# Kernel tuning notes

Measured on AMD Instinct MI355X. Metric: run time of the kernel, lower is better.

The kernel has to match this reference:

```python
import jax, jax.numpy as jnp
import numpy as np

DIM = 256
HEADS = 8
WS = 8            # window size
SHIFT = 4
MLP_HID = 1024
EPS = 1e-5
HEAD_DIM = DIM // HEADS
SCALE = HEAD_DIM ** -0.5
N = WS * WS       # tokens per window


def _rel_pos_index():
    coords = np.stack(np.meshgrid(np.arange(WS), np.arange(WS), indexing='ij'))  # [2,ws,ws]
    flat = coords.reshape(2, -1)                                                  # [2,N]
    rel = flat[:, :, None] - flat[:, None, :]                                     # [2,N,N]
    rel = rel.transpose(1, 2, 0)                                                  # [N,N,2]
    rel[:, :, 0] += WS - 1
    rel[:, :, 1] += WS - 1
    rel[:, :, 0] *= 2 * WS - 1
    return jnp.asarray(rel.sum(-1))                                               # [N,N] int

REL_IDX = _rel_pos_index()


def layernorm(x, g, b):
    mu = x.mean(-1, keepdims=True)
    var = ((x - mu) ** 2).mean(-1, keepdims=True)
    return (x - mu) * jax.lax.rsqrt(var + EPS) * g + b


def setup_inputs() -> dict:
    key = jax.random.key(0)
    ks = jax.random.split(key, 16)
    s = 0.02
    return {
        'x': jax.random.normal(ks[0], (16, 16384, DIM), jnp.float32),
        'qkv_w': jax.random.normal(ks[1], (DIM, 3 * DIM), jnp.float32) * s,
        'qkv_b': jnp.zeros((3 * DIM,), jnp.float32),
        'proj_w': jax.random.normal(ks[2], (DIM, DIM), jnp.float32) * s,
        'proj_b': jnp.zeros((DIM,), jnp.float32),
        'rpb_table': jax.random.normal(ks[3], ((2 * WS - 1) ** 2, HEADS), jnp.float32) * s,
        'ln1_g': jnp.ones((DIM,), jnp.float32),
        'ln1_b': jnp.zeros((DIM,), jnp.float32),
        'ln2_g': jnp.ones((DIM,), jnp.float32),
        'ln2_b': jnp.zeros((DIM,), jnp.float32),
        'mlp_w1': jax.random.normal(ks[4], (DIM, MLP_HID), jnp.float32) * s,
        'mlp_b1': jnp.zeros((MLP_HID,), jnp.float32),
        'mlp_w2': jax.random.normal(ks[5], (MLP_HID, DIM), jnp.float32) * s,
        'mlp_b2': jnp.zeros((DIM,), jnp.float32),
        'H': 128,
        'W': 128,
    }


def reference(x, qkv_w, qkv_b, proj_w, proj_b, rpb_table,
              ln1_g, ln1_b, ln2_g, ln2_b, mlp_w1, mlp_b1, mlp_w2, mlp_b2, H, W):
    B, L, C = x.shape
    shortcut = x

    h = layernorm(x, ln1_g, ln1_b).reshape(B, H, W, C)
    if SHIFT > 0:
        h = jnp.roll(h, (-SHIFT, -SHIFT), axis=(1, 2))

    # window partition: [B,H,W,C] -> [B*nW, N, C]
    h = h.reshape(B, H // WS, WS, W // WS, WS, C).transpose(0, 1, 3, 2, 4, 5)
    xw = h.reshape(-1, N, C)
    Bw = xw.shape[0]

    # window attention
    qkv = (xw @ qkv_w + qkv_b).reshape(Bw, N, 3, HEADS, HEAD_DIM)
    q, k, v = qkv[:, :, 0], qkv[:, :, 1], qkv[:, :, 2]        # [Bw,N,H,D]
    attn = jnp.einsum('bnhd,bmhd->bhnm', q, k) * SCALE         # [Bw,H,N,N]
    bias = rpb_table[REL_IDX.reshape(-1)].reshape(N, N, HEADS).transpose(2, 0, 1)
    attn = jax.nn.softmax(attn + bias[None], axis=-1)
    out = jnp.einsum('bhnm,bmhd->bnhd', attn, v).reshape(Bw, N, C)
    out = out @ proj_w + proj_b

    # window reverse
    out = out.reshape(B, H // WS, W // WS, WS, WS, C).transpose(0, 1, 3, 2, 4, 5).reshape(B, H, W, C)
    if SHIFT > 0:
        out = jnp.roll(out, (SHIFT, SHIFT), axis=(1, 2))
    out = out.reshape(B, L, C)

    h2 = layernorm(out, ln2_g, ln2_b)
    mlp = jax.nn.gelu(h2 @ mlp_w1 + mlp_b1, approximate=False) @ mlp_w2 + mlp_b2
    return shortcut + out + mlp
```

## Files before the change

kernel.cpp:

```cpp
#include <hip/hip_runtime.h>
#include <math.h>

typedef short bfrag __attribute__((ext_vector_type(8)));
typedef float ffrag __attribute__((ext_vector_type(4)));

#define MFMA16(a, b, c) __builtin_amdgcn_mfma_f32_16x16x32_bf16((a), (b), (c), 0, 0, 0)

__device__ __align__(16) unsigned short g_wt[786432];

__device__ __forceinline__ unsigned bf16b(float f) {
  unsigned u = __float_as_uint(f);
  return (u + 0x7FFFu + ((u >> 16) & 1u)) >> 16;
}
__device__ __forceinline__ unsigned pk2(float lo, float hi) {
  return bf16b(lo) | (bf16b(hi) << 16);
}

__global__ void conv_w(const float* __restrict__ qkv_w, const float* __restrict__ proj_w,
                       const float* __restrict__ w1, const float* __restrict__ w2) {
  const int idx = blockIdx.x * 256 + threadIdx.x;
  const float* src; int c, k2, C, K, ofs;
  if (idx < 98304)       { src = qkv_w;  C = 768;  K = 256;  c = idx % 768;  k2 = idx / 768;  ofs = 0; }
  else if (idx < 131072) { int i = idx - 98304;  src = proj_w; C = 256;  K = 256;  c = i % 256;  k2 = i / 256;  ofs = 196608; }
  else if (idx < 262144) { int i = idx - 131072; src = w1;     C = 1024; K = 256;  c = i % 1024; k2 = i / 1024; ofs = 262144; }
  else                   { int i = idx - 262144; src = w2;     C = 256;  K = 1024; c = i % 256;  k2 = i / 256;  ofs = 524288; }
  const float lo = src[(2 * k2) * C + c];
  const float hi = src[(2 * k2 + 1) * C + c];
  *(unsigned*)&g_wt[ofs + c * K + 2 * k2] = pk2(lo, hi);
}

__device__ __forceinline__ int swz(int row, int col, int C) {
  return row * (C * 2) + ((((col >> 3) ^ (row & 7)) << 4) + ((col & 7) << 1));
}

__device__ __forceinline__ bfrag ldfrag(const char* lds, int outer, int k0, int C) {
  const int l = threadIdx.x & 63;
  return *(const bfrag*)(lds + swz(outer + (l & 15), k0 + ((l >> 4) << 3), C));
}

template <int DSTROWB>
__device__ __forceinline__ void glds_stage(char* lds, const unsigned short* src,
                                           int srcRowShorts, int bytes) {
  const int wv = threadIdx.x >> 6, l = threadIdx.x & 63;
  for (int base = wv * 1024; base < bytes; base += 8192) {
    const int off = base + l * 16;
    const int row = off / DSTROWB;
    const int slot = (off % DSTROWB) >> 4;
    const int sslot = slot ^ (row & 7);
    const unsigned short* g = src + row * srcRowShorts + sslot * 8;
    __builtin_amdgcn_global_load_lds((const __attribute__((address_space(1))) void*)g,
                                     (__attribute__((address_space(3))) void*)(lds + base),
                                     16, 0, 0);
  }
}

__device__ __forceinline__ void ln_row_to_lds(char* dst, const float* __restrict__ src,
                                              const float* __restrict__ g,
                                              const float* __restrict__ bb, int r) {
  const int lane = threadIdx.x & 63;
  const float4 v = *(const float4*)(src + lane * 4);
  float s = v.x + v.y + v.z + v.w;
  #pragma unroll
  for (int o = 32; o; o >>= 1) s += __shfl_xor(s, o);
  const float mu = s * (1.f / 256.f);
  const float d0 = v.x - mu, d1 = v.y - mu, d2 = v.z - mu, d3 = v.w - mu;
  float q = d0 * d0 + d1 * d1 + d2 * d2 + d3 * d3;
  #pragma unroll
  for (int o = 32; o; o >>= 1) q += __shfl_xor(q, o);
  float rs = rsqrtf(q * (1.f / 256.f) + 1e-5f);
  rs = rs * (1.5f - 0.5f * (q * (1.f / 256.f) + 1e-5f) * rs * rs);
  const float4 g4 = *(const float4*)(g + lane * 4);
  const float4 b4 = *(const float4*)(bb + lane * 4);
  const int c = lane * 4;
  *(unsigned*)(dst + swz(r, c, 256)) = pk2(d0 * rs * g4.x + b4.x, d1 * rs * g4.y + b4.y);
  *(unsigned*)(dst + swz(r, c + 2, 256)) = pk2(d2 * rs * g4.z + b4.z, d3 * rs * g4.w + b4.w);
}

__global__ __launch_bounds__(512) void swin_attn(
    const float* __restrict__ x,
    const float* __restrict__ qkv_b, const float* __restrict__ proj_b,
    const float* __restrict__ rpb,
    const float* __restrict__ ln1g, const float* __restrict__ ln1b,
    float* __restrict__ outw)
{
  __shared__ __align__(16) char smem[147456];
  char* XW = smem;
  char* WS = smem + 32768;
  char* QL = smem + 49152;
  char* KL = smem + 81920;
  char* VT = smem + 114688;

  const int t = threadIdx.x;
  const int wv = t >> 6, l = t & 63;
  const int blk = blockIdx.x;
  const int b = blk >> 8, w = blk & 255;
  const int wi = w >> 4, wj = w & 15;

  #pragma unroll
  for (int i = 0; i < 8; ++i) {
    const int r = wv * 8 + i;
    const int ui = (wi * 8 + (r >> 3) + 4) & 127;
    const int uj = (wj * 8 + (r & 7) + 4) & 127;
    const long row = ((long)b << 14) + (ui << 7) + uj;
    ln_row_to_lds(XW, x + row * 256, ln1g, ln1b, r);
  }
  __syncthreads();

  const int MB = (wv >> 2) << 4;
  const int NB = (wv & 3) << 4;
  const float SC = 0.17677669529663687f;

  for (int ch = 0; ch < 24; ++ch) {
    glds_stage<512>(WS, g_wt + ch * 32 * 256, 256, 16384);
    __syncthreads();
    ffrag acc = {0.f, 0.f, 0.f, 0.f};
    #pragma unroll
    for (int ks = 0; ks < 8; ++ks) {
      const bfrag a = ldfrag(WS, MB, ks * 32, 256);
      const bfrag bb = ldfrag(XW, NB, ks * 32, 256);
      acc = MFMA16(a, bb, acc);
    }
    const int r = NB + (l & 15);
    const int cg = ch * 32 + MB + ((l >> 4) << 2);
    const float4 b4 = *(const float4*)(qkv_b + cg);
    float v0 = acc.x + b4.x, v1 = acc.y + b4.y, v2 = acc.z + b4.z, v3 = acc.w + b4.w;
    if (cg < 256) {
      v0 *= SC; v1 *= SC; v2 *= SC; v3 *= SC;
      *(unsigned*)(QL + swz(r, cg, 256)) = pk2(v0, v1);
      *(unsigned*)(QL + swz(r, cg + 2, 256)) = pk2(v2, v3);
    } else if (cg < 512) {
      const int c = cg - 256;
      *(unsigned*)(KL + swz(r, c, 256)) = pk2(v0, v1);
      *(unsigned*)(KL + swz(r, c + 2, 256)) = pk2(v2, v3);
    } else {
      const int c = cg - 512;
      *(unsigned short*)(VT + swz(c + 0, r, 64)) = (unsigned short)bf16b(v0);
      *(unsigned short*)(VT + swz(c + 1, r, 64)) = (unsigned short)bf16b(v1);
      *(unsigned short*)(VT + swz(c + 2, r, 64)) = (unsigned short)bf16b(v2);
      *(unsigned short*)(VT + swz(c + 3, r, 64)) = (unsigned short)bf16b(v3);
    }
    __syncthreads();
  }

  const int w4 = wv & 3;
  const int half = wv >> 2;
  for (int hp = 0; hp < 4; ++hp) {
    const int h = hp * 2 + half;
    char* PB = WS + half * 8192;
    const int hk = h * 32;

    const bfrag aq = ldfrag(QL, w4 * 16, hk, 256);
    ffrag s[4];
    #pragma unroll
    for (int nt = 0; nt < 4; ++nt) {
      const bfrag bk = ldfrag(KL, nt * 16, hk, 256);
      ffrag z = {0.f, 0.f, 0.f, 0.f};
      s[nt] = MFMA16(aq, bk, z);
    }
    const int colb = l & 15;
    const int rbase = w4 * 16 + ((l >> 4) << 2);
    float pr[4][4], mx[4], sm[4];
    #pragma unroll
    for (int reg = 0; reg < 4; ++reg) mx[reg] = -3e38f;
    #pragma unroll
    for (int nt = 0; nt < 4; ++nt) {
      #pragma unroll
      for (int reg = 0; reg < 4; ++reg) {
        const int rr = rbase + reg, cc = nt * 16 + colb;
        const int idx = ((rr >> 3) - (cc >> 3) + 7) * 15 + ((rr & 7) - (cc & 7) + 7);
        pr[nt][reg] = s[nt][reg] + rpb[idx * 8 + h];
        mx[reg] = fmaxf(mx[reg], pr[nt][reg]);
      }
    }
    #pragma unroll
    for (int reg = 0; reg < 4; ++reg) {
      #pragma unroll
      for (int o = 1; o < 16; o <<= 1) mx[reg] = fmaxf(mx[reg], __shfl_xor(mx[reg], o));
      sm[reg] = 0.f;
    }
    #pragma unroll
    for (int nt = 0; nt < 4; ++nt)
      #pragma unroll
      for (int reg = 0; reg < 4; ++reg) {
        pr[nt][reg] = __expf(pr[nt][reg] - mx[reg]);
        sm[reg] += pr[nt][reg];
      }
    #pragma unroll
    for (int reg = 0; reg < 4; ++reg) {
      #pragma unroll
      for (int o = 1; o < 16; o <<= 1) sm[reg] += __shfl_xor(sm[reg], o);
      sm[reg] = 1.f / sm[reg];
    }
    #pragma unroll
    for (int nt = 0; nt < 4; ++nt)
      #pragma unroll
      for (int reg = 0; reg < 4; ++reg)
        *(unsigned short*)(PB + swz(rbase + reg, nt * 16 + colb, 64)) =
            (unsigned short)bf16b(pr[nt][reg] * sm[reg]);
    __syncthreads();

    ffrag o0 = {0.f, 0.f, 0.f, 0.f}, o1 = {0.f, 0.f, 0.f, 0.f};
    #pragma unroll
    for (int ks = 0; ks < 2; ++ks) {
      const bfrag ap = ldfrag(PB, w4 * 16, ks * 32, 64);
      const bfrag bv0 = ldfrag(VT, hk, ks * 32, 64);
      const bfrag bv1 = ldfrag(VT, hk + 16, ks * 32, 64);
      o0 = MFMA16(ap, bv0, o0);
      o1 = MFMA16(ap, bv1, o1);
    }
    #pragma unroll
    for (int reg = 0; reg < 4; ++reg) {
      *(unsigned short*)(XW + swz(rbase + reg, hk + colb, 256)) = (unsigned short)bf16b(o0[reg]);
      *(unsigned short*)(XW + swz(rbase + reg, hk + 16 + colb, 256)) = (unsigned short)bf16b(o1[reg]);
    }
    __syncthreads();
  }

  for (int ch = 0; ch < 8; ++ch) {
    glds_stage<512>(WS, g_wt + 196608 + ch * 32 * 256, 256, 16384);
    __syncthreads();
    ffrag acc = {0.f, 0.f, 0.f, 0.f};
    #pragma unroll
    for (int ks = 0; ks < 8; ++ks) {
      const bfrag a = ldfrag(WS, MB, ks * 32, 256);
      const bfrag bo = ldfrag(XW, NB, ks * 32, 256);
      acc = MFMA16(a, bo, acc);
    }
    const int r = NB + (l & 15);
    const int c0 = ch * 32 + MB + ((l >> 4) << 2);
    const float4 pb4 = *(const float4*)(proj_b + c0);
    const int ui = (wi * 8 + (r >> 3) + 4) & 127;
    const int uj = (wj * 8 + (r & 7) + 4) & 127;
    const long row = ((long)b << 14) + (ui << 7) + uj;
    float4 o4;
    o4.x = acc.x + pb4.x; o4.y = acc.y + pb4.y;
    o4.z = acc.z + pb4.z; o4.w = acc.w + pb4.w;
    *(float4*)(outw + row * 256 + c0) = o4;
    __syncthreads();
  }
}

__global__ __launch_bounds__(512, 4) void swin_mlp(
    const float* __restrict__ x, const float* __restrict__ outw,
    const float* __restrict__ ln2g, const float* __restrict__ ln2b,
    const float* __restrict__ b1, const float* __restrict__ b2,
    float* __restrict__ y)
{
  __shared__ __align__(16) char smem[73728];
  char* H2 = smem;
  char* WS = smem + 32768;
  char* HD = smem + 65536;
  const int t = threadIdx.x, wv = t >> 6, l = t & 63;
  const long base = (long)blockIdx.x << 6;

  #pragma unroll
  for (int i = 0; i < 8; ++i) {
    const int r = wv * 8 + i;
    ln_row_to_lds(H2, outw + (base + r) * 256, ln2g, ln2b, r);
  }
  __syncthreads();

  const int mq = wv >> 1;
  const int nq = (wv & 1) << 1;

  ffrag acc2[2][4];
  {
    ffrag z = {0.f, 0.f, 0.f, 0.f};
    #pragma unroll
    for (int mt = 0; mt < 2; ++mt)
      #pragma unroll
      for (int nt = 0; nt < 4; ++nt) acc2[mt][nt] = z;
  }

  for (int ch = 0; ch < 16; ++ch) {
    glds_stage<512>(WS, g_wt + 262144 + ch * 64 * 256, 256, 32768);
    __syncthreads();
    ffrag a1[2];
    {
      ffrag z = {0.f, 0.f, 0.f, 0.f};
      a1[0] = z; a1[1] = z;
    }
    #pragma unroll
    for (int ks = 0; ks < 8; ++ks) {
      const bfrag a = ldfrag(WS, mq * 16, ks * 32, 256);
      const bfrag bb0 = ldfrag(H2, nq * 16, ks * 32, 256);
      const bfrag bb1 = ldfrag(H2, (nq + 1) * 16, ks * 32, 256);
      a1[0] = MFMA16(a, bb0, a1[0]);
      a1[1] = MFMA16(a, bb1, a1[1]);
    }
    __syncthreads();

    const int c0 = mq * 16 + ((l >> 4) << 2);
    const float4 b14 = *(const float4*)(b1 + ch * 64 + c0);
    #pragma unroll
    for (int nt = 0; nt < 2; ++nt) {
      const int rr = (nq + nt) * 16 + (l & 15);
      const float u0 = a1[nt][0] + b14.x, u1 = a1[nt][1] + b14.y;
      const float u2 = a1[nt][2] + b14.z, u3 = a1[nt][3] + b14.w;
      const float g0 = 0.5f * u0 * (1.f + erff(u0 * 0.70710678118654752f));
      const float g1 = 0.5f * u1 * (1.f + erff(u1 * 0.70710678118654752f));
      const float g2 = 0.5f * u2 * (1.f + erff(u2 * 0.70710678118654752f));
      const float g3 = 0.5f * u3 * (1.f + erff(u3 * 0.70710678118654752f));
      *(unsigned*)(HD + swz(rr, c0, 64)) = pk2(g0, g1);
      *(unsigned*)(HD + swz(rr, c0 + 2, 64)) = pk2(g2, g3);
    }
    glds_stage<128>(WS, g_wt + 524288 + ch * 64, 1024, 32768);
    __syncthreads();

    #pragma unroll
    for (int ks = 0; ks < 2; ++ks) {
      const bfrag am0 = ldfrag(WS, (wv * 2) * 16, ks * 32, 64);
      const bfrag am1 = ldfrag(WS, (wv * 2 + 1) * 16, ks * 32, 64);
      #pragma unroll
      for (int nt = 0; nt < 4; ++nt) {
        const bfrag bb = ldfrag(HD, nt * 16, ks * 32, 64);
        acc2[0][nt] = MFMA16(am0, bb, acc2[0][nt]);
        acc2[1][nt] = MFMA16(am1, bb, acc2[1][nt]);
      }
    }
    __syncthreads();
  }

  #pragma unroll
  for (int mt = 0; mt < 2; ++mt) {
    const int c0 = (wv * 2 + mt) * 16 + ((l >> 4) << 2);
    const float4 b24 = *(const float4*)(b2 + c0);
    #pragma unroll
    for (int nt = 0; nt < 4; ++nt) {
      const long row = base + nt * 16 + (l & 15);
      const float4 xv = *(const float4*)(x + row * 256 + c0);
      const float4 ov = *(const float4*)(outw + row * 256 + c0);
      float4 res;
      res.x = xv.x + ov.x + acc2[mt][nt][0] + b24.x;
      res.y = xv.y + ov.y + acc2[mt][nt][1] + b24.y;
      res.z = xv.z + ov.z + acc2[mt][nt][2] + b24.z;
      res.w = xv.w + ov.w + acc2[mt][nt][3] + b24.w;
      *(float4*)(y + row * 256 + c0) = res;
    }
  }
}

extern "C" void kernel_launch(void* const* d_in, const int* in_sizes, int n_in,
                              void* d_out, int out_size, void* d_ws, size_t ws_size,
                              hipStream_t stream) {
  (void)in_sizes; (void)n_in; (void)out_size; (void)ws_size;
  const float* x      = (const float*)d_in[0];
  const float* qkv_w  = (const float*)d_in[1];
  const float* qkv_b  = (const float*)d_in[2];
  const float* proj_w = (const float*)d_in[3];
  const float* proj_b = (const float*)d_in[4];
  const float* rpb    = (const float*)d_in[5];
  const float* ln1g   = (const float*)d_in[6];
  const float* ln1b   = (const float*)d_in[7];
  const float* ln2g   = (const float*)d_in[8];
  const float* ln2b   = (const float*)d_in[9];
  const float* b1     = (const float*)d_in[11];
  const float* w2     = (const float*)d_in[12];
  const float* b2     = (const float*)d_in[13];
  const float* w1     = (const float*)d_in[10];
  float* y    = (float*)d_out;
  float* outw = (float*)d_ws;

  hipLaunchKernelGGL(conv_w, dim3(1536), dim3(256), 0, stream, qkv_w, proj_w, w1, w2);
  hipLaunchKernelGGL(swin_attn, dim3(4096), dim3(512), 0, stream,
                     x, qkv_b, proj_b, rpb, ln1g, ln1b, outw);
  hipLaunchKernelGGL(swin_mlp, dim3(4096), dim3(512), 0, stream,
                     x, outw, ln2g, ln2b, b1, b2, y);
}
```

Baseline: 1.426 ms.

## Split fused window attention into LN1, QKV GEMM, attention core and projection kernels

```diff
diff --git a/kernel.cpp b/kernel.cpp
--- a/kernel.cpp
+++ b/kernel.cpp
@@ -14,6 +14,9 @@
 }
 __device__ __forceinline__ unsigned pk2(float lo, float hi) {
   return bf16b(lo) | (bf16b(hi) << 16);
+}
+__device__ __forceinline__ float bf2f(unsigned u) {
+  return __uint_as_float(u << 16);
 }
 
 __global__ void conv_w(const float* __restrict__ qkv_w, const float* __restrict__ proj_w,
@@ -32,10 +35,25 @@
 __device__ __forceinline__ int swz(int row, int col, int C) {
   return row * (C * 2) + ((((col >> 3) ^ (row & 7)) << 4) + ((col & 7) << 1));
 }
-
 __device__ __forceinline__ bfrag ldfrag(const char* lds, int outer, int k0, int C) {
   const int l = threadIdx.x & 63;
   return *(const bfrag*)(lds + swz(outer + (l & 15), k0 + ((l >> 4) << 3), C));
+}
+
+__device__ __forceinline__ void stage_tile(char* lds, const unsigned short* __restrict__ src,
+                                           long rowBase, int strideShorts, int kOfs) {
+  const int wv = threadIdx.x >> 6, l = threadIdx.x & 63;
+  #pragma unroll
+  for (int p = 0; p < 8; ++p) {
+    const int base = wv * 1024 + p * 8192;
+    const int off = base + l * 16;
+    const int row = off >> 9;
+    const int ss = ((off & 511) >> 4) ^ (row & 7);
+    const unsigned short* g = src + (rowBase + row) * (long)strideShorts + kOfs + ss * 8;
+    __builtin_amdgcn_global_load_lds((const __attribute__((address_space(1))) void*)g,
+                                     (__attribute__((address_space(3))) void*)(lds + base),
+                                     16, 0, 0);
+  }
 }
 
 template <int DSTROWB>
@@ -46,124 +64,188 @@
     const int off = base + l * 16;
     const int row = off / DSTROWB;
     const int slot = (off % DSTROWB) >> 4;
-    const int sslot = slot ^ (row & 7);
-    const unsigned short* g = src + row * srcRowShorts + sslot * 8;
+    const int ss = slot ^ (row & 7);
+    const unsigned short* g = src + row * srcRowShorts + ss * 8;
     __builtin_amdgcn_global_load_lds((const __attribute__((address_space(1))) void*)g,
                                      (__attribute__((address_space(3))) void*)(lds + base),
                                      16, 0, 0);
   }
 }
 
-__device__ __forceinline__ void ln_row_to_lds(char* dst, const float* __restrict__ src,
-                                              const float* __restrict__ g,
-                                              const float* __restrict__ bb, int r) {
-  const int lane = threadIdx.x & 63;
-  const float4 v = *(const float4*)(src + lane * 4);
-  float s = v.x + v.y + v.z + v.w;
+__device__ __forceinline__ void mm_core(const char* AX, const char* BW, ffrag acc[2][4]) {
+  const int wv = threadIdx.x >> 6;
+  const int rh = wv >> 2, cq = wv & 3;
+  #pragma unroll
+  for (int ks = 0; ks < 8; ++ks) {
+    const bfrag aw0 = ldfrag(BW, cq * 32, ks * 32, 256);
+    const bfrag aw1 = ldfrag(BW, cq * 32 + 16, ks * 32, 256);
+    #pragma unroll
+    for (int nt = 0; nt < 4; ++nt) {
+      const bfrag xb = ldfrag(AX, rh * 64 + nt * 16, ks * 32, 256);
+      acc[0][nt] = MFMA16(aw0, xb, acc[0][nt]);
+      acc[1][nt] = MFMA16(aw1, xb, acc[1][nt]);
+    }
+  }
+}
+
+__device__ __forceinline__ void ln_pack(float d0, float d1, float d2, float d3,
+                                        const float* g, const float* bb, int lane,
+                                        unsigned& o0, unsigned& o1) {
+  float s = d0 + d1 + d2 + d3;
   #pragma unroll
   for (int o = 32; o; o >>= 1) s += __shfl_xor(s, o);
   const float mu = s * (1.f / 256.f);
-  const float d0 = v.x - mu, d1 = v.y - mu, d2 = v.z - mu, d3 = v.w - mu;
+  d0 -= mu; d1 -= mu; d2 -= mu; d3 -= mu;
   float q = d0 * d0 + d1 * d1 + d2 * d2 + d3 * d3;
   #pragma unroll
   for (int o = 32; o; o >>= 1) q += __shfl_xor(q, o);
-  float rs = rsqrtf(q * (1.f / 256.f) + 1e-5f);
-  rs = rs * (1.5f - 0.5f * (q * (1.f / 256.f) + 1e-5f) * rs * rs);
+  const float vv = q * (1.f / 256.f) + 1e-5f;
+  float rs = rsqrtf(vv);
+  rs = rs * (1.5f - 0.5f * vv * rs * rs);
   const float4 g4 = *(const float4*)(g + lane * 4);
   const float4 b4 = *(const float4*)(bb + lane * 4);
-  const int c = lane * 4;
-  *(unsigned*)(dst + swz(r, c, 256)) = pk2(d0 * rs * g4.x + b4.x, d1 * rs * g4.y + b4.y);
-  *(unsigned*)(dst + swz(r, c + 2, 256)) = pk2(d2 * rs * g4.z + b4.z, d3 * rs * g4.w + b4.w);
-}
-
-__global__ __launch_bounds__(512) void swin_attn(
-    const float* __restrict__ x,
-    const float* __restrict__ qkv_b, const float* __restrict__ proj_b,
-    const float* __restrict__ rpb,
-    const float* __restrict__ ln1g, const float* __restrict__ ln1b,
-    float* __restrict__ outw)
-{
-  __shared__ __align__(16) char smem[147456];
-  char* XW = smem;
-  char* WS = smem + 32768;
-  char* QL = smem + 49152;
-  char* KL = smem + 81920;
-  char* VT = smem + 114688;
-
-  const int t = threadIdx.x;
-  const int wv = t >> 6, l = t & 63;
+  o0 = pk2(d0 * rs * g4.x + b4.x, d1 * rs * g4.y + b4.y);
+  o1 = pk2(d2 * rs * g4.z + b4.z, d3 * rs * g4.w + b4.w);
+}
+
+__global__ __launch_bounds__(512) void ln1_k(const float* __restrict__ x,
+    const float* __restrict__ g, const float* __restrict__ bb,
+    unsigned short* __restrict__ XB, long rowOfs) {
+  const int wv = threadIdx.x >> 6, l = threadIdx.x & 63;
+  const long lrow = (long)blockIdx.x * 8 + wv;
+  const float4 v = *(const float4*)(x + (rowOfs + lrow) * 256 + l * 4);
+  unsigned o0, o1;
+  ln_pack(v.x, v.y, v.z, v.w, g, bb, l, o0, o1);
+  unsigned short* dp = XB + lrow * 256 + l * 4;
+  *(unsigned*)dp = o0; *(unsigned*)(dp + 2) = o1;
+}
+
+__global__ __launch_bounds__(512) void gemm_qkv(const unsigned short* __restrict__ XB,
+    const float* __restrict__ qkv_b, unsigned short* __restrict__ QKV) {
+  __shared__ __align__(16) char smem[131072];
+  char* AX = smem; char* BW = smem + 65536;
+  const int mb = blockIdx.x, nb = blockIdx.y;
+  stage_tile(AX, XB, (long)mb * 128, 256, 0);
+  stage_tile(BW, g_wt, nb * 128, 256, 0);
+  __syncthreads();
+  ffrag acc[2][4];
+  #pragma unroll
+  for (int a = 0; a < 2; ++a)
+    #pragma unroll
+    for (int n = 0; n < 4; ++n) { ffrag z = {0.f, 0.f, 0.f, 0.f}; acc[a][n] = z; }
+  mm_core(AX, BW, acc);
+  const int l = threadIdx.x & 63, wv = threadIdx.x >> 6;
+  const int rh = wv >> 2, cq = wv & 3;
+  const float sc = (nb < 2) ? 0.17677669529663687f : 1.f;
+  #pragma unroll
+  for (int mt = 0; mt < 2; ++mt) {
+    const int cg = nb * 128 + cq * 32 + mt * 16 + ((l >> 4) << 2);
+    const float4 bq = *(const float4*)(qkv_b + cg);
+    #pragma unroll
+    for (int nt = 0; nt < 4; ++nt) {
+      const long row = (long)mb * 128 + rh * 64 + nt * 16 + (l & 15);
+      unsigned short* dp = QKV + row * 768 + cg;
+      *(unsigned*)dp       = pk2((acc[mt][nt][0] + bq.x) * sc, (acc[mt][nt][1] + bq.y) * sc);
+      *(unsigned*)(dp + 2) = pk2((acc[mt][nt][2] + bq.z) * sc, (acc[mt][nt][3] + bq.w) * sc);
+    }
+  }
+}
+
+__global__ __launch_bounds__(512) void gemm_proj(const unsigned short* __restrict__ O,
+    const float* __restrict__ proj_b, unsigned short* __restrict__ outw) {
+  __shared__ __align__(16) char smem[131072];
+  char* AX = smem; char* BW = smem + 65536;
+  const int mb = blockIdx.x, nb = blockIdx.y;
+  stage_tile(AX, O, (long)mb * 128, 256, 0);
+  stage_tile(BW, g_wt + 196608, nb * 128, 256, 0);
+  __syncthreads();
+  ffrag acc[2][4];
+  #pragma unroll
+  for (int a = 0; a < 2; ++a)
+    #pragma unroll
+    for (int n = 0; n < 4; ++n) { ffrag z = {0.f, 0.f, 0.f, 0.f}; acc[a][n] = z; }
+  mm_core(AX, BW, acc);
+  const int l = threadIdx.x & 63, wv = threadIdx.x >> 6;
+  const int rh = wv >> 2, cq = wv & 3;
+  #pragma unroll
+  for (int mt = 0; mt < 2; ++mt) {
+    const int cg = nb * 128 + cq * 32 + mt * 16 + ((l >> 4) << 2);
+    const float4 pb = *(const float4*)(proj_b + cg);
+    #pragma unroll
+    for (int nt = 0; nt < 4; ++nt) {
+      const long row = (long)mb * 128 + rh * 64 + nt * 16 + (l & 15);
+      unsigned short* dp = outw + row * 256 + cg;
+      *(unsigned*)dp       = pk2(acc[mt][nt][0] + pb.x, acc[mt][nt][1] + pb.y);
+      *(unsigned*)(dp + 2) = pk2(acc[mt][nt][2] + pb.z, acc[mt][nt][3] + pb.w);
+    }
+  }
+}
+
+__global__ __launch_bounds__(512, 4) void attn_core(const unsigned short* __restrict__ QKV,
+    const float* __restrict__ rpb, unsigned short* __restrict__ O, int bofs) {
+  __shared__ __align__(16) char smem[81920];
+  char* KL = smem;
+  char* VT = smem + 32768;
+  char* PB = smem + 65536;
+  const int t = threadIdx.x, wv = t >> 6, l = t & 63;
   const int blk = blockIdx.x;
   const int b = blk >> 8, w = blk & 255;
   const int wi = w >> 4, wj = w & 15;
-
-  #pragma unroll
-  for (int i = 0; i < 8; ++i) {
-    const int r = wv * 8 + i;
-    const int ui = (wi * 8 + (r >> 3) + 4) & 127;
-    const int uj = (wj * 8 + (r & 7) + 4) & 127;
-    const long row = ((long)b << 14) + (ui << 7) + uj;
-    ln_row_to_lds(XW, x + row * 256, ln1g, ln1b, r);
+  const int bi0 = wi * 8 + 4, bj0 = wj * 8 + 4;
+  const ffrag ZERO4 = {0.f, 0.f, 0.f, 0.f};
+
+  #define SROW(r) (((long)b << 14) + (((bi0 + ((r) >> 3)) & 127) << 7) + ((bj0 + ((r) & 7)) & 127))
+  #define GROW(r) (((long)(bofs + b) << 14) + (((bi0 + ((r) >> 3)) & 127) << 7) + ((bj0 + ((r) & 7)) & 127))
+
+  #pragma unroll
+  for (int p = 0; p < 4; ++p) {
+    const int base = wv * 1024 + p * 8192;
+    const int off = base + l * 16;
+    const int kv = off >> 9;
+    const int ss = ((off & 511) >> 4) ^ (kv & 7);
+    const unsigned short* g = QKV + SROW(kv) * 768 + 256 + ss * 8;
+    __builtin_amdgcn_global_load_lds((const __attribute__((address_space(1))) void*)g,
+                                     (__attribute__((address_space(3))) void*)(KL + base),
+                                     16, 0, 0);
+  }
+
+  {
+    const int rp = t & 31, dh = t >> 5;
+    const unsigned short* v0p = QKV + SROW(2 * rp) * 768 + 512 + dh * 16;
+    const unsigned short* v1p = QKV + SROW(2 * rp + 1) * 768 + 512 + dh * 16;
+    const bfrag a0 = *(const bfrag*)v0p, a1 = *(const bfrag*)(v0p + 8);
+    const bfrag c0 = *(const bfrag*)v1p, c1 = *(const bfrag*)(v1p + 8);
+    #pragma unroll
+    for (int j = 0; j < 8; ++j) {
+      const unsigned w0 = ((unsigned)(unsigned short)a0[j]) | (((unsigned)(unsigned short)c0[j]) << 16);
+      const unsigned w1 = ((unsigned)(unsigned short)a1[j]) | (((unsigned)(unsigned short)c1[j]) << 16);
+      *(unsigned*)(VT + swz(dh * 16 + j, 2 * rp, 64)) = w0;
+      *(unsigned*)(VT + swz(dh * 16 + 8 + j, 2 * rp, 64)) = w1;
+    }
   }
   __syncthreads();
 
-  const int MB = (wv >> 2) << 4;
-  const int NB = (wv & 3) << 4;
-  const float SC = 0.17677669529663687f;
-
-  for (int ch = 0; ch < 24; ++ch) {
-    glds_stage<512>(WS, g_wt + ch * 32 * 256, 256, 16384);
-    __syncthreads();
-    ffrag acc = {0.f, 0.f, 0.f, 0.f};
-    #pragma unroll
-    for (int ks = 0; ks < 8; ++ks) {
-      const bfrag a = ldfrag(WS, MB, ks * 32, 256);
-      const bfrag bb = ldfrag(XW, NB, ks * 32, 256);
-      acc = MFMA16(a, bb, acc);
-    }
-    const int r = NB + (l & 15);
-    const int cg = ch * 32 + MB + ((l >> 4) << 2);
-    const float4 b4 = *(const float4*)(qkv_b + cg);
-    float v0 = acc.x + b4.x, v1 = acc.y + b4.y, v2 = acc.z + b4.z, v3 = acc.w + b4.w;
-    if (cg < 256) {
-      v0 *= SC; v1 *= SC; v2 *= SC; v3 *= SC;
-      *(unsigned*)(QL + swz(r, cg, 256)) = pk2(v0, v1);
-      *(unsigned*)(QL + swz(r, cg + 2, 256)) = pk2(v2, v3);
-    } else if (cg < 512) {
-      const int c = cg - 256;
-      *(unsigned*)(KL + swz(r, c, 256)) = pk2(v0, v1);
-      *(unsigned*)(KL + swz(r, c + 2, 256)) = pk2(v2, v3);
-    } else {
-      const int c = cg - 512;
-      *(unsigned short*)(VT + swz(c + 0, r, 64)) = (unsigned short)bf16b(v0);
-      *(unsigned short*)(VT + swz(c + 1, r, 64)) = (unsigned short)bf16b(v1);
-      *(unsigned short*)(VT + swz(c + 2, r, 64)) = (unsigned short)bf16b(v2);
-      *(unsigned short*)(VT + swz(c + 3, r, 64)) = (unsigned short)bf16b(v3);
-    }
-    __syncthreads();
-  }
-
-  const int w4 = wv & 3;
-  const int half = wv >> 2;
-  for (int hp = 0; hp < 4; ++hp) {
-    const int h = hp * 2 + half;
-    char* PB = WS + half * 8192;
+  const int qt = wv & 3, hh = wv >> 2;
+  char* myPB = PB + wv * 2048;
+  const int colb = l & 15;
+  const int rbase = qt * 16 + ((l >> 4) << 2);
+
+  for (int i = 0; i < 4; ++i) {
+    const int h = 2 * i + hh;
     const int hk = h * 32;
-
-    const bfrag aq = ldfrag(QL, w4 * 16, hk, 256);
+    const int qr = qt * 16 + (l & 15);
+    const bfrag aq = *(const bfrag*)(QKV + SROW(qr) * 768 + hk + ((l >> 4) << 3));
     ffrag s[4];
     #pragma unroll
     for (int nt = 0; nt < 4; ++nt) {
       const bfrag bk = ldfrag(KL, nt * 16, hk, 256);
-      ffrag z = {0.f, 0.f, 0.f, 0.f};
-      s[nt] = MFMA16(aq, bk, z);
-    }
-    const int colb = l & 15;
-    const int rbase = w4 * 16 + ((l >> 4) << 2);
+      s[nt] = MFMA16(aq, bk, ZERO4);
+    }
     float pr[4][4], mx[4], sm[4];
     #pragma unroll
     for (int reg = 0; reg < 4; ++reg) mx[reg] = -3e38f;
     #pragma unroll
-    for (int nt = 0; nt < 4; ++nt) {
+    for (int nt = 0; nt < 4; ++nt)
       #pragma unroll
       for (int reg = 0; reg < 4; ++reg) {
         const int rr = rbase + reg, cc = nt * 16 + colb;
@@ -171,7 +253,6 @@
         pr[nt][reg] = s[nt][reg] + rpb[idx * 8 + h];
         mx[reg] = fmaxf(mx[reg], pr[nt][reg]);
       }
-    }
     #pragma unroll
     for (int reg = 0; reg < 4; ++reg) {
       #pragma unroll
@@ -195,14 +276,13 @@
     for (int nt = 0; nt < 4; ++nt)
       #pragma unroll
       for (int reg = 0; reg < 4; ++reg)
-        *(unsigned short*)(PB + swz(rbase + reg, nt * 16 + colb, 64)) =
+        *(unsigned short*)(myPB + swz(((l >> 4) << 2) + reg, nt * 16 + colb, 64)) =
             (unsigned short)bf16b(pr[nt][reg] * sm[reg]);
-    __syncthreads();
-
-    ffrag o0 = {0.f, 0.f, 0.f, 0.f}, o1 = {0.f, 0.f, 0.f, 0.f};
+
+    ffrag o0 = ZERO4, o1 = ZERO4;
     #pragma unroll
     for (int ks = 0; ks < 2; ++ks) {
-      const bfrag ap = ldfrag(PB, w4 * 16, ks * 32, 64);
+      const bfrag ap = ldfrag(myPB, 0, ks * 32, 64);
       const bfrag bv0 = ldfrag(VT, hk, ks * 32, 64);
       const bfrag bv1 = ldfrag(VT, hk + 16, ks * 32, 64);
       o0 = MFMA16(ap, bv0, o0);
@@ -210,38 +290,17 @@
     }
     #pragma unroll
     for (int reg = 0; reg < 4; ++reg) {
-      *(unsigned short*)(XW + swz(rbase + reg, hk + colb, 256)) = (unsigned short)bf16b(o0[reg]);
-      *(unsigned short*)(XW + swz(rbase + reg, hk + 16 + colb, 256)) = (unsigned short)bf16b(o1[reg]);
-    }
-    __syncthreads();
-  }
-
-  for (int ch = 0; ch < 8; ++ch) {
-    glds_stage<512>(WS, g_wt + 196608 + ch * 32 * 256, 256, 16384);
-    __syncthreads();
-    ffrag acc = {0.f, 0.f, 0.f, 0.f};
-    #pragma unroll
-    for (int ks = 0; ks < 8; ++ks) {
-      const bfrag a = ldfrag(WS, MB, ks * 32, 256);
-      const bfrag bo = ldfrag(XW, NB, ks * 32, 256);
-      acc = MFMA16(a, bo, acc);
-    }
-    const int r = NB + (l & 15);
-    const int c0 = ch * 32 + MB + ((l >> 4) << 2);
-    const float4 pb4 = *(const float4*)(proj_b + c0);
-    const int ui = (wi * 8 + (r >> 3) + 4) & 127;
-    const int uj = (wj * 8 + (r & 7) + 4) & 127;
-    const long row = ((long)b << 14) + (ui << 7) + uj;
-    float4 o4;
-    o4.x = acc.x + pb4.x; o4.y = acc.y + pb4.y;
-    o4.z = acc.z + pb4.z; o4.w = acc.w + pb4.w;
-    *(float4*)(outw + row * 256 + c0) = o4;
-    __syncthreads();
-  }
+      const long orow = GROW(rbase + reg);
+      O[orow * 256 + hk + colb] = (unsigned short)bf16b(o0[reg]);
+      O[orow * 256 + hk + 16 + colb] = (unsigned short)bf16b(o1[reg]);
+    }
+  }
+  #undef SROW
+  #undef GROW
 }
 
 __global__ __launch_bounds__(512, 4) void swin_mlp(
-    const float* __restrict__ x, const float* __restrict__ outw,
+    const float* __restrict__ x, const unsigned short* __restrict__ outw,
     const float* __restrict__ ln2g, const float* __restrict__ ln2b,
     const float* __restrict__ b1, const float* __restrict__ b2,
     float* __restrict__ y)
@@ -256,30 +315,28 @@
   #pragma unroll
   for (int i = 0; i < 8; ++i) {
     const int r = wv * 8 + i;
-    ln_row_to_lds(H2, outw + (base + r) * 256, ln2g, ln2b, r);
+    const uint2 raw = *(const uint2*)(outw + (base + r) * 256 + l * 4);
+    unsigned o0, o1;
+    ln_pack(bf2f(raw.x & 0xFFFFu), bf2f(raw.x >> 16), bf2f(raw.y & 0xFFFFu), bf2f(raw.y >> 16),
+            ln2g, ln2b, l, o0, o1);
+    *(unsigned*)(H2 + swz(r, l * 4, 256)) = o0;
+    *(unsigned*)(H2 + swz(r, l * 4 + 2, 256)) = o1;
   }
   __syncthreads();
 
-  const int mq = wv >> 1;
-  const int nq = (wv & 1) << 1;
+  const int mq = wv >> 1, nq = (wv & 1) << 1;
 
   ffrag acc2[2][4];
-  {
-    ffrag z = {0.f, 0.f, 0.f, 0.f};
-    #pragma unroll
-    for (int mt = 0; mt < 2; ++mt)
-      #pragma unroll
-      for (int nt = 0; nt < 4; ++nt) acc2[mt][nt] = z;
-  }
+  #pragma unroll
+  for (int mt = 0; mt < 2; ++mt)
+    #pragma unroll
+    for (int nt = 0; nt < 4; ++nt) { ffrag z = {0.f, 0.f, 0.f, 0.f}; acc2[mt][nt] = z; }
 
   for (int ch = 0; ch < 16; ++ch) {
     glds_stage<512>(WS, g_wt + 262144 + ch * 64 * 256, 256, 32768);
     __syncthreads();
     ffrag a1[2];
-    {
-      ffrag z = {0.f, 0.f, 0.f, 0.f};
-      a1[0] = z; a1[1] = z;
-    }
+    { ffrag z = {0.f, 0.f, 0.f, 0.f}; a1[0] = z; a1[1] = z; }
     #pragma unroll
     for (int ks = 0; ks < 8; ++ks) {
       const bfrag a = ldfrag(WS, mq * 16, ks * 32, 256);
@@ -329,12 +386,12 @@
     for (int nt = 0; nt < 4; ++nt) {
       const long row = base + nt * 16 + (l & 15);
       const float4 xv = *(const float4*)(x + row * 256 + c0);
-      const float4 ov = *(const float4*)(outw + row * 256 + c0);
+      const uint2 ov = *(const uint2*)(outw + row * 256 + c0);
       float4 res;
-      res.x = xv.x + ov.x + acc2[mt][nt][0] + b24.x;
-      res.y = xv.y + ov.y + acc2[mt][nt][1] + b24.y;
-      res.z = xv.z + ov.z + acc2[mt][nt][2] + b24.z;
-      res.w = xv.w + ov.w + acc2[mt][nt][3] + b24.w;
+      res.x = acc2[mt][nt][0] + b24.x + xv.x + bf2f(ov.x & 0xFFFFu);
+      res.y = acc2[mt][nt][1] + b24.y + xv.y + bf2f(ov.x >> 16);
+      res.z = acc2[mt][nt][2] + b24.z + xv.z + bf2f(ov.y & 0xFFFFu);
+      res.w = acc2[mt][nt][3] + b24.w + xv.w + bf2f(ov.y >> 16);
       *(float4*)(y + row * 256 + c0) = res;
     }
   }
@@ -354,16 +411,26 @@
   const float* ln1b   = (const float*)d_in[7];
   const float* ln2g   = (const float*)d_in[8];
   const float* ln2b   = (const float*)d_in[9];
+  const float* w1     = (const float*)d_in[10];
   const float* b1     = (const float*)d_in[11];
   const float* w2     = (const float*)d_in[12];
   const float* b2     = (const float*)d_in[13];
-  const float* w1     = (const float*)d_in[10];
-  float* y    = (float*)d_out;
-  float* outw = (float*)d_ws;
+  float* y = (float*)d_out;
+  char* ws = (char*)d_ws;
+
+  unsigned short* XB   = (unsigned short*)(ws);
+  unsigned short* QKV  = (unsigned short*)(ws + 33554432);
+  unsigned short* Obuf = (unsigned short*)(ws + 134217728);
+  unsigned short* outw = (unsigned short*)(ws);
 
   hipLaunchKernelGGL(conv_w, dim3(1536), dim3(256), 0, stream, qkv_w, proj_w, w1, w2);
-  hipLaunchKernelGGL(swin_attn, dim3(4096), dim3(512), 0, stream,
-                     x, qkv_b, proj_b, rpb, ln1g, ln1b, outw);
+  for (int g = 0; g < 4; ++g) {
+    hipLaunchKernelGGL(ln1_k, dim3(8192), dim3(512), 0, stream,
+                       x, ln1g, ln1b, XB, (long)g * 65536);
+    hipLaunchKernelGGL(gemm_qkv, dim3(512, 6), dim3(512), 0, stream, XB, qkv_b, QKV);
+    hipLaunchKernelGGL(attn_core, dim3(1024), dim3(512), 0, stream, QKV, rpb, Obuf, g * 4);
+  }
+  hipLaunchKernelGGL(gemm_proj, dim3(2048, 2), dim3(512), 0, stream, Obuf, proj_b, outw);
   hipLaunchKernelGGL(swin_mlp, dim3(4096), dim3(512), 0, stream,
                      x, outw, ln2g, ln2b, b1, b2, y);
 }
```

After: 1.301 ms. 1.1x faster.
